# Kernel tuning notes

Hardware: AMD Instinct MI355X
Metric: run time of the kernel (lower is better)

The kernel has to match this reference:

```python
import jax, jax.numpy as jnp
import numpy as np

# hyperparameters matching init_kwargs
SIGMA_COLOR = 1.0 / (1.0 * 1.0 * 2)   # 1/(2*sigma_color^2), sigma_color=1.0
SIGMA_SPACE = 1.0 / (1.0 * 1.0 * 2)   # 1/(2*sigma_space^2), sigma_space=1.0
WINDOW_SIZE = 1                        # 3x3 window
LP = 0.8                               # p_small (Lp norm from paper)
P_LARGE = 2.0                          # p_large for flat regions
C1 = 1.0
C2 = 1.0
EPS = 1e-8


def _window_diffs(img, w):
    """Stack img - shifted(img) over all (2w+1)^2 offsets, reflection padded.
    Faithful to the torch indexing: offset index = (x+w) + (y+w)*(2w+1),
    x applied to the height axis, y to the width axis (H must equal W).
    Returns [B, (2w+1)^2, C, H, W]."""
    B, C, H, W = img.shape
    p = jnp.pad(img, ((0, 0), (0, 0), (w, w), (w, w)), mode='reflect')
    outs = []
    for y in range(-w, w + 1):
        for x in range(-w, w + 1):
            outs.append(img - p[:, :, w + x: w + x + H, w + y: w + y + W])
    return jnp.stack(outs, axis=1)


def _spatial_weights(w, sigma_space, dtype):
    ws = []
    for y in range(-w, w + 1):
        for x in range(-w, w + 1):
            ws.append(np.exp(-sigma_space * (x * x + y * y)))
    return jnp.asarray(np.array(ws, dtype=np.float32), dtype=dtype)  # [(2w+1)^2]


def _edge_response(img):
    """Simple gradient-magnitude edge response, summed over channels. [B,H,W]"""
    p = jnp.pad(img, ((0, 0), (0, 0), (1, 1), (1, 1)), mode='reflect')
    dx = img - p[:, :, 2:, 1:-1]   # vertical neighbor diff
    dy = img - p[:, :, 1:-1, 2:]   # horizontal neighbor diff
    return (dx * dx + dy * dy).sum(axis=1)


def setup_inputs() -> dict:
    key = jax.random.key(0)
    k1, k2 = jax.random.split(key)
    original_images = jax.random.normal(k1, (8, 3, 512, 512), dtype=jnp.float32)
    smooth_images = jax.random.normal(k2, (8, 3, 512, 512), dtype=jnp.float32)
    return {"original_images": original_images, "smooth_images": smooth_images}


def reference(original_images, smooth_images):
    w = WINDOW_SIZE
    # 1. |Ti - Tj| over the (2w+1)^2 window  -> [B, K, C, H, W]
    d = jnp.abs(_window_diffs(smooth_images, w))

    # 2. bilateral color weight wr from original images (3x3 window, hardcoded
    #    window_size=1 in the torch module)  -> [B, 9, 1, H, W]
    diff_o = _window_diffs(original_images, 1)
    wr = jnp.exp((-SIGMA_COLOR * diff_o * diff_o).sum(axis=2, keepdims=True))

    # spatial Gaussian weight ws per offset -> broadcast [1, K, 1, 1, 1]
    ws = _spatial_weights(w, SIGMA_SPACE, d.dtype)[None, :, None, None, None]

    # 3. binary masks from edge responses
    e_orig = _edge_response(original_images)   # [B, H, W]
    e_smooth = _edge_response(smooth_images)
    use_large = ((e_orig < C1) & (e_smooth - e_orig > C2))
    mask_large = use_large[:, None, None, :, :].astype(d.dtype)  # [B,1,1,H,W]

    # masked weighted Lp loss (p_large on flat regions with ws, p_small with wr)
    term_large = ws * jnp.power(d + EPS, P_LARGE)
    term_small = wr * jnp.power(d + EPS, LP)
    loss = jnp.mean(mask_large * term_large + (1.0 - mask_large) * term_small)
    return loss
```

## Files before the change

### kernel.cpp

```cpp
#include <hip/hip_runtime.h>

__device__ __forceinline__ float fexp2(float x) { return __builtin_amdgcn_exp2f(x); }
__device__ __forceinline__ float flog2(float x) { return __builtin_amdgcn_logf(x); }

struct Node { float o0, o1, o2, s0, s1, s2; };

__device__ __forceinline__ float pair_core(const Node& I, const Node& J,
                                           float wsm, float wl, float wsd)
{
    float d0 = I.o0 - J.o0, d1 = I.o1 - J.o1, d2 = I.o2 - J.o2;
    float sO = fmaf(d0, d0, fmaf(d1, d1, d2 * d2));
    float t0 = fabsf(I.s0 - J.s0) + 1e-8f;
    float t1 = fabsf(I.s1 - J.s1) + 1e-8f;
    float t2 = fabsf(I.s2 - J.s2) + 1e-8f;
    float ps = fexp2(0.8f * flog2(t0)) + fexp2(0.8f * flog2(t1)) + fexp2(0.8f * flog2(t2));
    float wr = fexp2(-0.72134752044448169f * sO);
    float sq = fmaf(t0, t0, fmaf(t1, t1, t2 * t2));
    return fmaf(wsm * wr, ps, wl * wsd * sq);
}

__device__ __forceinline__ float pixel_border(
    const Node& C, const Node& E, const Node& S, const Node& SE, const Node& SW,
    float mi, float mE, float mS, float mSE, float mSW, int h, int w)
{
    float aE = (w == 0)   ? 2.f : 1.f, bE = (w == 510) ? 2.f : 1.f;
    float aS = (h == 0)   ? 2.f : 1.f, bS = (h == 510) ? 2.f : 1.f;
    float aW = (w == 511) ? 2.f : 1.f, bW = (w == 1)   ? 2.f : 1.f;
    bool  vE = (w <= 510), vS = (h <= 510);
    bool  vD = vS && vE,   vW = vS && (w >= 1);
    float cEf = vE ? aE : 0.f,      cEb = vE ? bE : 0.f;
    float cSf = vS ? aS : 0.f,      cSb = vS ? bS : 0.f;
    float cDf = vD ? aS * aE : 0.f, cDb = vD ? bS * bE : 0.f;
    float cWf = vW ? aS * aW : 0.f, cWb = vW ? bS * bW : 0.f;

    float a = fmaf(mi, 3e-16f - 1.1943215e-6f, 1.1943215e-6f);
    a += pair_core(C, E,  fmaf(cEf, -mi, cEf) + fmaf(cEb, -mE,  cEb), fmaf(cEf, mi, cEb * mE),  0.60653065971263342f);
    a += pair_core(C, S,  fmaf(cSf, -mi, cSf) + fmaf(cSb, -mS,  cSb), fmaf(cSf, mi, cSb * mS),  0.60653065971263342f);
    a += pair_core(C, SE, fmaf(cDf, -mi, cDf) + fmaf(cDb, -mSE, cDb), fmaf(cDf, mi, cDb * mSE), 0.36787944117144233f);
    a += pair_core(C, SW, fmaf(cWf, -mi, cWf) + fmaf(cWb, -mSW, cWb), fmaf(cWf, mi, cWb * mSW), 0.36787944117144233f);
    return a;
}

__device__ __forceinline__ void load_row(float R[6][5], const float* const pb[6],
                                         int row, int cm1, int c0, int c2, int c3)
{
    int gh = row > 511 ? 1022 - row : row;
    #pragma unroll
    for (int p = 0; p < 6; ++p) {
        const float* g = pb[p] + (gh << 9);
        R[p][0] = g[cm1];
        float2 v = *(const float2*)(g + c0);
        R[p][1] = v.x; R[p][2] = v.y;
        R[p][3] = g[c2];
        R[p][4] = g[c3];
    }
}

__device__ __forceinline__ void mask_row(float M[4], const float B_[6][5], const float C_[6][5])
{
    #pragma unroll
    for (int j = 0; j < 4; ++j) {
        float eo = 0.f, es = 0.f;
        #pragma unroll
        for (int p = 0; p < 3; ++p) {
            float a = B_[p][j];
            float d1 = a - C_[p][j], d2 = a - B_[p][j + 1];
            eo += d1 * d1 + d2 * d2;
            float s = B_[p + 3][j];
            float f1 = s - C_[p + 3][j], f2 = s - B_[p + 3][j + 1];
            es += f1 * f1 + f2 * f2;
        }
        M[j] = (eo < 1.f && es - eo > 1.f) ? 1.f : 0.f;
    }
}

__device__ __forceinline__ Node mknode(const float R[6][5], int i)
{
    Node n; n.o0 = R[0][i]; n.o1 = R[1][i]; n.o2 = R[2][i];
    n.s0 = R[3][i]; n.s1 = R[4][i]; n.s2 = R[5][i]; return n;
}

#define MSTEP(A_, B_, C_, N_, S_, DOLOAD_)                                        \
    {                                                                             \
        if (DOLOAD_) load_row(N_, pb, h0 + (S_) + 3, cm1, c0, c2, c3);            \
        float mN[4]; mask_row(mN, B_, C_);                                        \
        const int hh = h0 + (S_);                                                 \
        acc += pixel_border(mknode(A_,1), mknode(A_,2), mknode(B_,1),             \
                            mknode(B_,2), mknode(B_,0),                           \
                            mC[1], mC[2], mN[1], mN[2], mN[0], hh, c0);           \
        acc += pixel_border(mknode(A_,2), mknode(A_,3), mknode(B_,2),             \
                            mknode(B_,3), mknode(B_,1),                           \
                            mC[2], mC[3], mN[2], mN[3], mN[1], hh, c0 + 1);       \
        mC[0] = mN[0]; mC[1] = mN[1]; mC[2] = mN[2]; mC[3] = mN[3];               \
    }

__global__ __launch_bounds__(256, 2) void smooth_loss_kernel(
    const float* __restrict__ orig, const float* __restrict__ smo,
    float* __restrict__ out)
{
    const int tid  = threadIdx.x;
    const int bid  = blockIdx.x;
    const int b    = bid >> 6;
    const int band = bid & 63;
    const int h0   = band << 3;
    const int c0   = tid << 1;

    const int cm1 = (c0 == 0) ? 1 : c0 - 1;
    const int c2  = (c0 + 2 > 511) ? 1022 - (c0 + 2) : c0 + 2;
    const int c3  = (c0 + 3 > 511) ? 1022 - (c0 + 3) : c0 + 3;

    const float* pb[6];
    #pragma unroll
    for (int p = 0; p < 3; ++p) {
        pb[p]     = orig + ((b * 3 + p) << 18);
        pb[p + 3] = smo  + ((b * 3 + p) << 18);
    }

    float D0[6][5], D1[6][5], D2[6][5], D3[6][5];
    float mC[4];
    float acc = 0.f;

    load_row(D0, pb, h0,     cm1, c0, c2, c3);
    load_row(D1, pb, h0 + 1, cm1, c0, c2, c3);
    load_row(D2, pb, h0 + 2, cm1, c0, c2, c3);
    mask_row(mC, D0, D1);

    MSTEP(D0, D1, D2, D3, 0, 1)
    MSTEP(D1, D2, D3, D0, 1, 1)
    MSTEP(D2, D3, D0, D1, 2, 1)
    MSTEP(D3, D0, D1, D2, 3, 1)
    MSTEP(D0, D1, D2, D3, 4, 1)
    MSTEP(D1, D2, D3, D0, 5, 1)
    MSTEP(D2, D3, D0, D1, 6, 1)
    MSTEP(D3, D0, D1, D2, 7, 0)

    acc *= (1.0f / 56623104.0f);

    #pragma unroll
    for (int o = 32; o > 0; o >>= 1)
        acc += __shfl_down(acc, o, 64);

    __shared__ float wsum[4];
    const int lane = tid & 63;
    const int wid  = tid >> 6;
    if (lane == 0) wsum[wid] = acc;
    __syncthreads();
    if (tid == 0)
        atomicAdd(out, wsum[0] + wsum[1] + wsum[2] + wsum[3]);
}

extern "C" void kernel_launch(void* const* d_in, const int* in_sizes, int n_in,
                              void* d_out, int out_size, void* d_ws, size_t ws_size,
                              hipStream_t stream) {
    const float* orig = (const float*)d_in[0];
    const float* smo  = (const float*)d_in[1];
    float* out = (float*)d_out;

    (void)hipMemsetAsync(out, 0, sizeof(float), stream);
    smooth_loss_kernel<<<512, 256, 0, stream>>>(orig, smo, out);
}
```

Baseline: 33.85 us.

## Split work to one column per thread and add border-free fast path

Each thread now handles a single column instead of two, and the grid doubles to 1024 blocks with launch bounds raised to 4 blocks per SM, which shrinks per-thread register state and increases parallelism. Wavefronts that touch no image border take a fast path with simplified mask weights instead of the per-pair reflection coefficient logic. The costs are extra redundant neighbor loads and mask recomputation per pixel, plus scalar loads replacing the float2 load.

```diff
diff --git a/kernel.cpp b/kernel.cpp
--- a/kernel.cpp
+++ b/kernel.cpp
@@ -17,6 +17,18 @@
     float wr = fexp2(-0.72134752044448169f * sO);
     float sq = fmaf(t0, t0, fmaf(t1, t1, t2 * t2));
     return fmaf(wsm * wr, ps, wl * wsd * sq);
+}
+
+__device__ __forceinline__ float pixel_fast(
+    const Node& C, const Node& E, const Node& S, const Node& SE, const Node& SW,
+    float mi, float mE, float mS, float mSE, float mSW)
+{
+    float a = fmaf(mi, 3e-16f - 1.1943215e-6f, 1.1943215e-6f);
+    a += pair_core(C, E,  2.f - mi - mE,  mi + mE,  0.60653065971263342f);
+    a += pair_core(C, S,  2.f - mi - mS,  mi + mS,  0.60653065971263342f);
+    a += pair_core(C, SE, 2.f - mi - mSE, mi + mSE, 0.36787944117144233f);
+    a += pair_core(C, SW, 2.f - mi - mSW, mi + mSW, 0.36787944117144233f);
+    return a;
 }
 
 __device__ __forceinline__ float pixel_border(
@@ -41,25 +53,21 @@
     return a;
 }
 
-__device__ __forceinline__ void load_row(float R[6][5], const float* const pb[6],
-                                         int row, int cm1, int c0, int c2, int c3)
+__device__ __forceinline__ void load_row(float R[6][4], const float* const pb[6],
+                                         int row, int cm1, int c, int cp1, int cp2)
 {
-    int gh = row > 511 ? 1022 - row : row;
+    const int rb = (row > 511 ? 1022 - row : row) << 9;
     #pragma unroll
     for (int p = 0; p < 6; ++p) {
-        const float* g = pb[p] + (gh << 9);
-        R[p][0] = g[cm1];
-        float2 v = *(const float2*)(g + c0);
-        R[p][1] = v.x; R[p][2] = v.y;
-        R[p][3] = g[c2];
-        R[p][4] = g[c3];
+        const float* g = pb[p] + rb;
+        R[p][0] = g[cm1]; R[p][1] = g[c]; R[p][2] = g[cp1]; R[p][3] = g[cp2];
     }
 }
 
-__device__ __forceinline__ void mask_row(float M[4], const float B_[6][5], const float C_[6][5])
+__device__ __forceinline__ void mask3(float M[3], const float B_[6][4], const float C_[6][4])
 {
     #pragma unroll
-    for (int j = 0; j < 4; ++j) {
+    for (int j = 0; j < 3; ++j) {
         float eo = 0.f, es = 0.f;
         #pragma unroll
         for (int p = 0; p < 3; ++p) {
@@ -74,7 +82,7 @@
     }
 }
 
-__device__ __forceinline__ Node mknode(const float R[6][5], int i)
+__device__ __forceinline__ Node mk(const float R[6][4], int i)
 {
     Node n; n.o0 = R[0][i]; n.o1 = R[1][i]; n.o2 = R[2][i];
     n.s0 = R[3][i]; n.s1 = R[4][i]; n.s2 = R[5][i]; return n;
@@ -82,32 +90,38 @@
 
 #define MSTEP(A_, B_, C_, N_, S_, DOLOAD_)                                        \
     {                                                                             \
-        if (DOLOAD_) load_row(N_, pb, h0 + (S_) + 3, cm1, c0, c2, c3);            \
-        float mN[4]; mask_row(mN, B_, C_);                                        \
-        const int hh = h0 + (S_);                                                 \
-        acc += pixel_border(mknode(A_,1), mknode(A_,2), mknode(B_,1),             \
-                            mknode(B_,2), mknode(B_,0),                           \
-                            mC[1], mC[2], mN[1], mN[2], mN[0], hh, c0);           \
-        acc += pixel_border(mknode(A_,2), mknode(A_,3), mknode(B_,2),             \
-                            mknode(B_,3), mknode(B_,1),                           \
-                            mC[2], mC[3], mN[2], mN[3], mN[1], hh, c0 + 1);       \
-        mC[0] = mN[0]; mC[1] = mN[1]; mC[2] = mN[2]; mC[3] = mN[3];               \
+        if (DOLOAD_) load_row(N_, pb, h0 + (S_) + 3, cm1, c, cp1, cp2);           \
+        float mN[3]; mask3(mN, B_, C_);                                           \
+        if (wborder) {                                                            \
+            acc += pixel_border(mk(A_,1), mk(A_,2), mk(B_,1), mk(B_,2), mk(B_,0), \
+                                mC[1], mC[2], mN[1], mN[2], mN[0], h0 + (S_), c); \
+        } else {                                                                  \
+            acc += pixel_fast(mk(A_,1), mk(A_,2), mk(B_,1), mk(B_,2), mk(B_,0),   \
+                              mC[1], mC[2], mN[1], mN[2], mN[0]);                 \
+        }                                                                         \
+        mC[0] = mN[0]; mC[1] = mN[1]; mC[2] = mN[2];                              \
     }
 
-__global__ __launch_bounds__(256, 2) void smooth_loss_kernel(
+__global__ __launch_bounds__(256, 4) void smooth_loss_kernel(
     const float* __restrict__ orig, const float* __restrict__ smo,
     float* __restrict__ out)
 {
     const int tid  = threadIdx.x;
     const int bid  = blockIdx.x;
-    const int b    = bid >> 6;
-    const int band = bid & 63;
+    const int b    = bid >> 7;
+    const int rem  = bid & 127;
+    const int band = rem >> 1;
+    const int half = rem & 1;
     const int h0   = band << 3;
-    const int c0   = tid << 1;
+    const int c    = (half << 8) | tid;
 
-    const int cm1 = (c0 == 0) ? 1 : c0 - 1;
-    const int c2  = (c0 + 2 > 511) ? 1022 - (c0 + 2) : c0 + 2;
-    const int c3  = (c0 + 3 > 511) ? 1022 - (c0 + 3) : c0 + 3;
+    const int cm1 = (c == 0)   ? 1   : c - 1;
+    const int cp1 = (c == 511) ? 510 : c + 1;
+    const int cp2 = (c >= 510) ? 1022 - (c + 2) : c + 2;
+
+    const int trow = band;
+    const int wc   = (half << 8) | (tid & 192);
+    const bool wborder = (trow == 0) | (trow == 63) | (wc == 0) | (wc == 448);
 
     const float* pb[6];
     #pragma unroll
@@ -116,14 +130,14 @@
         pb[p + 3] = smo  + ((b * 3 + p) << 18);
     }
 
-    float D0[6][5], D1[6][5], D2[6][5], D3[6][5];
-    float mC[4];
+    float D0[6][4], D1[6][4], D2[6][4], D3[6][4];
+    float mC[3];
     float acc = 0.f;
 
-    load_row(D0, pb, h0,     cm1, c0, c2, c3);
-    load_row(D1, pb, h0 + 1, cm1, c0, c2, c3);
-    load_row(D2, pb, h0 + 2, cm1, c0, c2, c3);
-    mask_row(mC, D0, D1);
+    load_row(D0, pb, h0,     cm1, c, cp1, cp2);
+    load_row(D1, pb, h0 + 1, cm1, c, cp1, cp2);
+    load_row(D2, pb, h0 + 2, cm1, c, cp1, cp2);
+    mask3(mC, D0, D1);
 
     MSTEP(D0, D1, D2, D3, 0, 1)
     MSTEP(D1, D2, D3, D0, 1, 1)
@@ -157,5 +171,5 @@
     float* out = (float*)d_out;
 
     (void)hipMemsetAsync(out, 0, sizeof(float), stream);
-    smooth_loss_kernel<<<512, 256, 0, stream>>>(orig, smo, out);
+    smooth_loss_kernel<<<1024, 256, 0, stream>>>(orig, smo, out);
 }
```

After: 91.20 us. 2.69x slower.
